# Optimization experiments

Hardware: AMD Instinct MI355X
Metric: run time of the kernel (lower is better)

The kernel has to match this reference:

```python
import jax, jax.numpy as jnp
import numpy as np

E = 320000   # num edges / messages
N = 10000    # num target nodes (dim_size)
C = 256      # in_channels == out_channels


def setup_inputs() -> dict:
    key = jax.random.key(0)
    k1, k2, k3, k4, k5, k6 = jax.random.split(key, 6)
    s = 1.0 / np.sqrt(C)  # torch Linear default init bound
    return {
        "from_tensor": jax.random.normal(k1, (E, C), dtype=jnp.float32),
        "to_index": jax.random.randint(k2, (E,), 0, N),
        "dim_size": N,
        "W1": jax.random.uniform(k3, (C, C), jnp.float32, -s, s),
        "b1": jax.random.uniform(k4, (C,), jnp.float32, -s, s),
        "W2": jax.random.uniform(k5, (C, C), jnp.float32, -s, s),
        "b2": jax.random.uniform(k6, (C,), jnp.float32, -s, s),
    }


def reference(from_tensor, to_index, dim_size, W1, b1, W2, b2):
    # InterMessage with transform_scatter=True, num_layers=2, reduction='mean':
    # message = MLP(from_tensor); out = scatter_mean(message, to_index, dim_size)
    m = jax.nn.relu(from_tensor @ W1 + b1)          # [E, C]
    m = jax.nn.relu(m @ W2 + b2)                    # [E, C]
    sums = jax.ops.segment_sum(m, to_index, num_segments=dim_size)  # [N, C]
    cnt = jax.ops.segment_sum(jnp.ones((m.shape[0], 1), m.dtype), to_index,
                              num_segments=dim_size)                # [N, 1]
    # scatter-mean: empty segments produce 0 (matches torch_scatter 'mean')
    return jnp.where(cnt > 0, sums / jnp.maximum(cnt, 1.0), 0.0)
```

## Files before the change

kernel.cpp:

```cpp
#include <hip/hip_runtime.h>

#define NUM_E 320000
#define NUM_N 10000

typedef __attribute__((ext_vector_type(8))) short bf16x8;
typedef __attribute__((ext_vector_type(4))) float f32x4;

__device__ __forceinline__ short f2bf(float f) {
  unsigned u = __builtin_bit_cast(unsigned, f);
  u += 0x7FFFu + ((u >> 16) & 1u);
  return (short)(u >> 16);
}

__global__ void combo_k(const float* __restrict__ W1, const float* __restrict__ W2,
                        short* __restrict__ Wp, const int* __restrict__ idx,
                        int* __restrict__ cnt, float* __restrict__ out) {
  int b = blockIdx.x;
  int t = threadIdx.x;
  if (b < 640) {
    int base = b * 256 + t;
#pragma unroll
    for (int k = 0; k < 4; ++k) {
      int f4 = base + k * 163840;
      if (f4 < 640000) reinterpret_cast<float4*>(out)[f4] = make_float4(0, 0, 0, 0);
    }
  } else if (b < 1890) {
    int e = (b - 640) * 256 + t;
    if (e < NUM_E) atomicAdd(&cnt[idx[e]], 1);
  } else {
    int gid = (b - 1890) * 256 + t;
    const float* W = (gid & 8192) ? W2 : W1;
    int r = gid & 8191;
    short* dst = Wp + (gid >> 13) * 65536 + r * 8;
    int j = r >> 9;
    int s = (r >> 6) & 7;
    int lane = r & 63;
    int n = j * 16 + (lane & 15);
    int k0 = s * 32 + (lane >> 4) * 8;
    short tmp[8];
#pragma unroll
    for (int e = 0; e < 8; ++e) tmp[e] = f2bf(W[(k0 + e) * 256 + n]);
#pragma unroll
    for (int e = 0; e < 8; ++e) dst[e] = tmp[e];
  }
}

__global__ void scan_k(const int* __restrict__ cnt, int* __restrict__ fill,
                       float* __restrict__ inv) {
  __shared__ int part[256];
  int t = threadIdx.x;
  int base = t * 40;
  int local[40];
  int s = 0;
#pragma unroll
  for (int i = 0; i < 40; ++i) {
    int n = base + i;
    int c = (n < NUM_N) ? cnt[n] : 0;
    local[i] = s;
    s += c;
  }
  part[t] = s;
  __syncthreads();
  for (int off = 1; off < 256; off <<= 1) {
    int tmp = 0;
    if (t >= off) tmp = part[t - off];
    __syncthreads();
    if (t >= off) part[t] += tmp;
    __syncthreads();
  }
  int ebase = (t == 0) ? 0 : part[t - 1];
#pragma unroll
  for (int i = 0; i < 40; ++i) {
    int n = base + i;
    if (n < NUM_N) {
      fill[n] = ebase + local[i];
      int c = cnt[n];
      inv[n] = (c > 0) ? 1.0f / (float)c : 0.0f;
    }
  }
}

__global__ void scatter_k(const int* __restrict__ idx, int* __restrict__ fill,
                          int* __restrict__ sorted) {
  int e = blockIdx.x * 256 + threadIdx.x;
  if (e < NUM_E) {
    int ix = idx[e];
    int pos = atomicAdd(&fill[ix], 1);
    sorted[pos] = e;
  }
}

__global__ __launch_bounds__(256, 4) void fused_mlp_gather(
    const float* __restrict__ X, const int* __restrict__ idx,
    const int* __restrict__ sorted,
    const short* __restrict__ Wp1, const short* __restrict__ Wp2,
    const float* __restrict__ b1, const float* __restrict__ b2,
    const float* __restrict__ inv, float* __restrict__ out) {
  __shared__ __align__(16) short Xl[64][264];
  __shared__ int idxl[64];
  __shared__ int se[64];
  __shared__ int segLo[64];
  __shared__ int segN[64];
  __shared__ int nsegS;

  const int tid = threadIdx.x;
  const int wave = tid >> 6;
  const int lane = tid & 63;
  const int q = lane >> 4;
  const int m = lane & 15;
  const int row0 = blockIdx.x * 64;

  if (tid < 64) {
    int e = sorted[row0 + tid];
    se[tid] = e;
    idxl[tid] = idx[e];
  }
  __syncthreads();

  for (int i = tid; i < 64 * 64; i += 256) {
    int r = i >> 6, c4 = i & 63;
    float4 v = reinterpret_cast<const float4*>(X + (size_t)se[r] * 256)[c4];
    unsigned long long packed =
        (unsigned long long)(unsigned short)f2bf(v.x) |
        ((unsigned long long)(unsigned short)f2bf(v.y) << 16) |
        ((unsigned long long)(unsigned short)f2bf(v.z) << 32) |
        ((unsigned long long)(unsigned short)f2bf(v.w) << 48);
    *reinterpret_cast<unsigned long long*>(&Xl[r][c4 * 4]) = packed;
  }
  __syncthreads();

  if (wave == 0) {
    bool flag = (lane == 0) || (idxl[lane] != idxl[lane - 1]);
    unsigned long long mask = __ballot(flag);
    if (lane == 0) nsegS = (int)__popcll(mask);
    if (flag) {
      int sidx = (int)__popcll(mask & ((1ull << lane) - 1ull));
      segLo[sidx] = lane;
      segN[sidx] = idxl[lane];
    }
  }

  f32x4 acc[4][4];
#pragma unroll
  for (int mi = 0; mi < 4; ++mi)
#pragma unroll
    for (int nj = 0; nj < 4; ++nj) acc[mi][nj] = (f32x4)0.0f;

#pragma unroll
  for (int s = 0; s < 8; ++s) {
    bf16x8 a[4], b[4];
#pragma unroll
    for (int mi = 0; mi < 4; ++mi)
      a[mi] = *reinterpret_cast<const bf16x8*>(&Xl[mi * 16 + m][s * 32 + q * 8]);
#pragma unroll
    for (int nj = 0; nj < 4; ++nj)
      b[nj] = *reinterpret_cast<const bf16x8*>(
          Wp1 + (size_t)(((wave * 4 + nj) * 8 + s) * 64 + lane) * 8);
#pragma unroll
    for (int mi = 0; mi < 4; ++mi)
#pragma unroll
      for (int nj = 0; nj < 4; ++nj)
        acc[mi][nj] = __builtin_amdgcn_mfma_f32_16x16x32_bf16(a[mi], b[nj],
                                                              acc[mi][nj], 0, 0, 0);
  }
  __syncthreads();

  float bias1[4];
#pragma unroll
  for (int nj = 0; nj < 4; ++nj) bias1[nj] = b1[wave * 64 + nj * 16 + m];
#pragma unroll
  for (int mi = 0; mi < 4; ++mi)
#pragma unroll
    for (int nj = 0; nj < 4; ++nj)
#pragma unroll
      for (int r4 = 0; r4 < 4; ++r4) {
        float v = fmaxf(acc[mi][nj][r4] + bias1[nj], 0.0f);
        Xl[mi * 16 + q * 4 + r4][wave * 64 + nj * 16 + m] = f2bf(v);
      }
  __syncthreads();

#pragma unroll
  for (int mi = 0; mi < 4; ++mi)
#pragma unroll
    for (int nj = 0; nj < 4; ++nj) acc[mi][nj] = (f32x4)0.0f;

#pragma unroll
  for (int s = 0; s < 8; ++s) {
    bf16x8 a[4], b[4];
#pragma unroll
    for (int mi = 0; mi < 4; ++mi)
      a[mi] = *reinterpret_cast<const bf16x8*>(&Xl[mi * 16 + m][s * 32 + q * 8]);
#pragma unroll
    for (int nj = 0; nj < 4; ++nj)
      b[nj] = *reinterpret_cast<const bf16x8*>(
          Wp2 + (size_t)(((wave * 4 + nj) * 8 + s) * 64 + lane) * 8);
#pragma unroll
    for (int mi = 0; mi < 4; ++mi)
#pragma unroll
      for (int nj = 0; nj < 4; ++nj)
        acc[mi][nj] = __builtin_amdgcn_mfma_f32_16x16x32_bf16(a[mi], b[nj],
                                                              acc[mi][nj], 0, 0, 0);
  }

  float bias2[4];
#pragma unroll
  for (int nj = 0; nj < 4; ++nj) bias2[nj] = b2[wave * 64 + nj * 16 + m];
#pragma unroll
  for (int mi = 0; mi < 4; ++mi)
#pragma unroll
    for (int nj = 0; nj < 4; ++nj)
#pragma unroll
      for (int r4 = 0; r4 < 4; ++r4)
        acc[mi][nj][r4] = fmaxf(acc[mi][nj][r4] + bias2[nj], 0.0f);

  int nseg = nsegS;
  for (int s = 0; s < nseg; ++s) {
    int lo = segLo[s];
    int hi = (s + 1 < nseg) ? segLo[s + 1] : 64;
    int node = segN[s];
    float sum[4] = {0.0f, 0.0f, 0.0f, 0.0f};
#pragma unroll
    for (int mi = 0; mi < 4; ++mi)
#pragma unroll
      for (int r4 = 0; r4 < 4; ++r4) {
        int row = mi * 16 + q * 4 + r4;
        float msk = (row >= lo && row < hi) ? 1.0f : 0.0f;
#pragma unroll
        for (int nj = 0; nj < 4; ++nj) sum[nj] = fmaf(msk, acc[mi][nj][r4], sum[nj]);
      }
    float scale = inv[node];
#pragma unroll
    for (int nj = 0; nj < 4; ++nj) {
      float v = sum[nj];
      v += __shfl_xor(v, 16, 64);
      v += __shfl_xor(v, 32, 64);
      if (q == 0 && v != 0.0f)
        atomicAdd(&out[(size_t)node * 256 + wave * 64 + nj * 16 + m], v * scale);
    }
  }
}

extern "C" void kernel_launch(void* const* d_in, const int* in_sizes, int n_in,
                              void* d_out, int out_size, void* d_ws, size_t ws_size,
                              hipStream_t stream) {
  const float* X   = (const float*)d_in[0];
  const int*   idx = (const int*)d_in[1];
  const float* W1  = (const float*)d_in[3];
  const float* b1  = (const float*)d_in[4];
  const float* W2  = (const float*)d_in[5];
  const float* b2  = (const float*)d_in[6];
  float* out = (float*)d_out;

  char* ws = (char*)d_ws;
  short* Wp     = (short*)(ws);
  int*   cnt    = (int*)(ws + 262144);
  int*   fill   = (int*)(ws + 303104);
  float* inv    = (float*)(ws + 344064);
  int*   sorted = (int*)(ws + 385024);

  hipMemsetAsync(cnt, 0, NUM_N * sizeof(int), stream);
  combo_k<<<1954, 256, 0, stream>>>(W1, W2, Wp, idx, cnt, out);
  scan_k<<<1, 256, 0, stream>>>(cnt, fill, inv);
  scatter_k<<<(NUM_E + 255) / 256, 256, 0, stream>>>(idx, fill, sorted);
  fused_mlp_gather<<<NUM_E / 64, 256, 0, stream>>>(
      X, idx, sorted, Wp, Wp + 65536, b1, b2, inv, out);
}
```

Baseline: 586.2 us.

## Merge preprocessing kernels into one cooperative kernel with padded counters

Replaces the memset plus the combo, scan and scatter kernels with a single cooperative kernel that uses grid syncs between phases. The scan becomes a parallel two-level scan across 40 blocks instead of a single-block serial scan. The count and fill counters are padded to 32 ints each to cut atomic contention and false sharing, and the sorted index buffer reuses the count array. The bf16 packing in the gather is also changed to use a perm instruction. It trades several launch gaps for five grid-wide barriers, and the cooperative launch needs all 1024 blocks to be resident at once.

After: 1.118 ms. 90.8% more time.

```diff
diff --git a/kernel.cpp b/kernel.cpp
--- a/kernel.cpp
+++ b/kernel.cpp
@@ -1,7 +1,11 @@
 #include <hip/hip_runtime.h>
+#include <hip/hip_cooperative_groups.h>
+
+namespace cg = cooperative_groups;
 
 #define NUM_E 320000
 #define NUM_N 10000
+#define PADC 32
 
 typedef __attribute__((ext_vector_type(8))) short bf16x8;
 typedef __attribute__((ext_vector_type(4))) float f32x4;
@@ -12,26 +16,35 @@
   return (short)(u >> 16);
 }
 
-__global__ void combo_k(const float* __restrict__ W1, const float* __restrict__ W2,
-                        short* __restrict__ Wp, const int* __restrict__ idx,
-                        int* __restrict__ cnt, float* __restrict__ out) {
-  int b = blockIdx.x;
-  int t = threadIdx.x;
-  if (b < 640) {
-    int base = b * 256 + t;
-#pragma unroll
-    for (int k = 0; k < 4; ++k) {
-      int f4 = base + k * 163840;
-      if (f4 < 640000) reinterpret_cast<float4*>(out)[f4] = make_float4(0, 0, 0, 0);
-    }
-  } else if (b < 1890) {
-    int e = (b - 640) * 256 + t;
-    if (e < NUM_E) atomicAdd(&cnt[idx[e]], 1);
-  } else {
-    int gid = (b - 1890) * 256 + t;
-    const float* W = (gid & 8192) ? W2 : W1;
-    int r = gid & 8191;
-    short* dst = Wp + (gid >> 13) * 65536 + r * 8;
+__device__ __forceinline__ unsigned pack2bf(float x, float y) {
+  unsigned ux = __builtin_bit_cast(unsigned, x);
+  unsigned uy = __builtin_bit_cast(unsigned, y);
+  ux += 0x7FFFu + ((ux >> 16) & 1u);
+  uy += 0x7FFFu + ((uy >> 16) & 1u);
+  return __builtin_amdgcn_perm(uy, ux, 0x07060302u);
+}
+
+__global__ __launch_bounds__(256, 4) void prep_k(
+    const float* __restrict__ W1, const float* __restrict__ W2,
+    short* __restrict__ Wp, const int* __restrict__ idx,
+    int* cntA ,
+    int* __restrict__ fillP, float* __restrict__ inv,
+    int* __restrict__ blockSum, int* __restrict__ chunkOff,
+    float* __restrict__ out) {
+  __shared__ int sc[256];
+  cg::grid_group grid = cg::this_grid();
+  const int t = threadIdx.x;
+  const int b = blockIdx.x;
+  const int gtid = b * 256 + t;
+  const int gsz = gridDim.x * 256;
+
+  for (int i = gtid; i < 640000; i += gsz)
+    reinterpret_cast<float4*>(out)[i] = make_float4(0.f, 0.f, 0.f, 0.f);
+  for (int i = gtid; i < NUM_N * PADC; i += gsz) cntA[i] = 0;
+  if (gtid < 16384) {
+    const float* W = (gtid & 8192) ? W2 : W1;
+    int r = gtid & 8191;
+    short* dst = Wp + (gtid >> 13) * 65536 + r * 8;
     int j = r >> 9;
     int s = (r >> 6) & 7;
     int lane = r & 63;
@@ -43,50 +56,46 @@
 #pragma unroll
     for (int e = 0; e < 8; ++e) dst[e] = tmp[e];
   }
-}
-
-__global__ void scan_k(const int* __restrict__ cnt, int* __restrict__ fill,
-                       float* __restrict__ inv) {
-  __shared__ int part[256];
-  int t = threadIdx.x;
-  int base = t * 40;
-  int local[40];
-  int s = 0;
-#pragma unroll
-  for (int i = 0; i < 40; ++i) {
-    int n = base + i;
-    int c = (n < NUM_N) ? cnt[n] : 0;
-    local[i] = s;
-    s += c;
-  }
-  part[t] = s;
-  __syncthreads();
-  for (int off = 1; off < 256; off <<= 1) {
-    int tmp = 0;
-    if (t >= off) tmp = part[t - off];
+  grid.sync();
+
+  for (int e = gtid; e < NUM_E; e += gsz) atomicAdd(&cntA[idx[e] * PADC], 1);
+  grid.sync();
+
+  if (b < 40) {
+    int n = b * 256 + t;
+    int c = (n < NUM_N) ? cntA[n * PADC] : 0;
+    sc[t] = c;
     __syncthreads();
-    if (t >= off) part[t] += tmp;
-    __syncthreads();
-  }
-  int ebase = (t == 0) ? 0 : part[t - 1];
-#pragma unroll
-  for (int i = 0; i < 40; ++i) {
-    int n = base + i;
+    for (int off = 1; off < 256; off <<= 1) {
+      int v = (t >= off) ? sc[t - off] : 0;
+      __syncthreads();
+      sc[t] += v;
+      __syncthreads();
+    }
     if (n < NUM_N) {
-      fill[n] = ebase + local[i];
-      int c = cnt[n];
+      fillP[n * PADC] = sc[t] - c;
       inv[n] = (c > 0) ? 1.0f / (float)c : 0.0f;
     }
-  }
-}
-
-__global__ void scatter_k(const int* __restrict__ idx, int* __restrict__ fill,
-                          int* __restrict__ sorted) {
-  int e = blockIdx.x * 256 + threadIdx.x;
-  if (e < NUM_E) {
+    if (t == 255) blockSum[b] = sc[255];
+  }
+  grid.sync();
+
+  if (gtid == 0) {
+    int s = 0;
+    for (int i = 0; i < 40; ++i) { chunkOff[i] = s; s += blockSum[i]; }
+  }
+  grid.sync();
+
+  if (b < 40) {
+    int n = b * 256 + t;
+    if (n < NUM_N) fillP[n * PADC] += chunkOff[b];
+  }
+  grid.sync();
+
+  for (int e = gtid; e < NUM_E; e += gsz) {
     int ix = idx[e];
-    int pos = atomicAdd(&fill[ix], 1);
-    sorted[pos] = e;
+    int pos = atomicAdd(&fillP[ix * PADC], 1);
+    cntA[pos] = e;
   }
 }
 
@@ -119,13 +128,11 @@
 
   for (int i = tid; i < 64 * 64; i += 256) {
     int r = i >> 6, c4 = i & 63;
-    float4 v = reinterpret_cast<const float4*>(X + (size_t)se[r] * 256)[c4];
-    unsigned long long packed =
-        (unsigned long long)(unsigned short)f2bf(v.x) |
-        ((unsigned long long)(unsigned short)f2bf(v.y) << 16) |
-        ((unsigned long long)(unsigned short)f2bf(v.z) << 32) |
-        ((unsigned long long)(unsigned short)f2bf(v.w) << 48);
-    *reinterpret_cast<unsigned long long*>(&Xl[r][c4 * 4]) = packed;
+    const float4 v = reinterpret_cast<const float4*>(X + (size_t)se[r] * 256)[c4];
+    uint2 p;
+    p.x = pack2bf(v.x, v.y);
+    p.y = pack2bf(v.z, v.w);
+    *reinterpret_cast<uint2*>(&Xl[r][c4 * 4]) = p;
   }
   __syncthreads();
 
@@ -252,16 +259,19 @@
   float* out = (float*)d_out;
 
   char* ws = (char*)d_ws;
-  short* Wp     = (short*)(ws);
-  int*   cnt    = (int*)(ws + 262144);
-  int*   fill   = (int*)(ws + 303104);
-  float* inv    = (float*)(ws + 344064);
-  int*   sorted = (int*)(ws + 385024);
-
-  hipMemsetAsync(cnt, 0, NUM_N * sizeof(int), stream);
-  combo_k<<<1954, 256, 0, stream>>>(W1, W2, Wp, idx, cnt, out);
-  scan_k<<<1, 256, 0, stream>>>(cnt, fill, inv);
-  scatter_k<<<(NUM_E + 255) / 256, 256, 0, stream>>>(idx, fill, sorted);
+  short* Wp       = (short*)(ws);
+  int*   cntA     = (int*)(ws + 262144);
+  int*   fillP    = (int*)(ws + 1542144);
+  float* inv      = (float*)(ws + 2822144);
+  int*   blockSum = (int*)(ws + 2862144);
+  int*   chunkOff = (int*)(ws + 2862400);
+  int*   sorted   = cntA;
+
+  void* args[] = {(void*)&W1, (void*)&W2, (void*)&Wp, (void*)&idx,
+                  (void*)&cntA, (void*)&fillP, (void*)&inv,
+                  (void*)&blockSum, (void*)&chunkOff, (void*)&out};
+  hipLaunchCooperativeKernel((void*)prep_k, dim3(1024), dim3(256), args, 0, stream);
+
   fused_mlp_gather<<<NUM_E / 64, 256, 0, stream>>>(
       X, idx, sorted, Wp, Wp + 65536, b1, b2, inv, out);
 }
```
